# Optimization experiments

Hardware: AMD Instinct MI355X
Metric: run time of the kernel (lower is better)

## Reference

```python
import jax, jax.numpy as jnp
import numpy as np
from jax import lax

T, B, H, HID = 1024, 64, 512, 512
EPS = 1e-5


def _lstm_scan(xs, Wx, Wh, b):
    # xs: [T, B, H] time-major; returns hidden states [T, B, HID]
    bsz = xs.shape[1]
    c0 = jnp.zeros((bsz, Wh.shape[0]), xs.dtype)
    h0 = jnp.zeros_like(c0)

    def step(carry, x):
        c, h = carry
        z = x @ Wx + h @ Wh + b  # [B, 4*HID]
        i, f, g, o = jnp.split(z, 4, axis=-1)  # flax gate order i, f, g, o
        c = jax.nn.sigmoid(f) * c + jax.nn.sigmoid(i) * jnp.tanh(g)
        h = jax.nn.sigmoid(o) * jnp.tanh(c)
        return (c, h), h

    _, hs = lax.scan(step, (c0, h0), xs)
    return hs


def _flip_sequences(x_bth, lengths):
    # x_bth: [B, T, H]; keep padding at the end while reversing valid prefix.
    max_len = x_bth.shape[1]
    return jax.vmap(lambda x, l: jnp.flip(jnp.roll(x, max_len - l, axis=0), axis=0))(
        x_bth, lengths)


def setup_inputs() -> dict:
    key = jax.random.key(0)
    ks = jax.random.split(key, 12)
    inputs = jax.random.normal(ks[0], (T, B, H), jnp.float32)
    lengths = jax.random.randint(ks[1], (B,), T // 2, T + 1).astype(jnp.int32)
    t_idx = jnp.arange(T)[:, None]
    mask = (t_idx < lengths[None, :]).astype(jnp.float32).reshape(T * B, 1)
    # BatchNorm params
    scale = 1.0 + 0.1 * jax.random.normal(ks[2], (H,), jnp.float32)
    bias = 0.1 * jax.random.normal(ks[3], (H,), jnp.float32)
    sx = 1.0 / np.sqrt(H)
    sh = 1.0 / np.sqrt(HID)
    Wx_f = sx * jax.random.normal(ks[4], (H, 4 * HID), jnp.float32)
    Wh_f = sh * jax.random.normal(ks[5], (HID, 4 * HID), jnp.float32)
    b_f = jnp.zeros((4 * HID,), jnp.float32)
    Wx_b = sx * jax.random.normal(ks[6], (H, 4 * HID), jnp.float32)
    Wh_b = sh * jax.random.normal(ks[7], (HID, 4 * HID), jnp.float32)
    b_b = jnp.zeros((4 * HID,), jnp.float32)
    return {
        "inputs": inputs, "lengths": lengths, "mask": mask,
        "scale": scale, "bias": bias,
        "Wx_f": Wx_f, "Wh_f": Wh_f, "b_f": b_f,
        "Wx_b": Wx_b, "Wh_b": Wh_b, "b_b": b_b,
        "training": 1,
    }


def reference(inputs, lengths, mask, scale, bias,
              Wx_f, Wh_f, b_f, Wx_b, Wh_b, b_b, training):
    t, n, h = inputs.shape
    x = inputs.reshape(t * n, h)
    if training:
        # masked batch statistics (matches flax BatchNorm override)
        non_zeros = jnp.sum(mask, axis=0)  # [1]
        mean = jnp.sum(x, axis=0) / non_zeros  # [H]
        mean2 = jnp.sum(lax.square(x), axis=0) / non_zeros
        var = jnp.maximum(0.0, mean2 - lax.square(mean))
    else:
        mean = jnp.zeros((h,), jnp.float32)
        var = jnp.ones((h,), jnp.float32)
    y = (x - mean) * lax.rsqrt(var + EPS) * scale + bias
    y = (y * mask).reshape(t, n, h)  # [T, B, H]

    # forward direction
    fwd = _lstm_scan(y, Wx_f, Wh_f, b_f)  # [T, B, HID]
    # backward direction on length-aware flipped inputs
    rev_in = _flip_sequences(y.transpose(1, 0, 2), lengths).transpose(1, 0, 2)
    bwd = _lstm_scan(rev_in, Wx_b, Wh_b, b_b)
    bwd = _flip_sequences(bwd.transpose(1, 0, 2), lengths).transpose(1, 0, 2)
    return fwd + bwd  # [T, B, HID]
```

## Files before the change

### kernel.cpp

```cpp
#include <hip/hip_runtime.h>
#include <math.h>

#define T_DIM 1024
#define B_DIM 64
#define H_DIM 512
#define HID   512
#define EPS_F 1e-5f

#define WS_SUM    0
#define WS_SUMSQ  512
#define WS_A      1024
#define WS_C0     1536
#define WS_HBUF   4096
#define WS_CBUF   (4096 + 131072)
#define WS_XZ     (4096 + 131072 + 65536)
#define WS_END    (WS_XZ + 524288)

__device__ __forceinline__ float sigf(float v) {
    return 1.0f / (1.0f + __expf(-v));
}

__global__ void stats_kernel(const float* __restrict__ x, float* __restrict__ ws) {
    int col = blockIdx.x * 256 + threadIdx.x;
    int row0 = blockIdx.y * 512;
    float s = 0.f, s2 = 0.f;
    for (int r = 0; r < 512; ++r) {
        float v = x[(size_t)(row0 + r) * H_DIM + col];
        s += v;
        s2 += v * v;
    }
    atomicAdd(&ws[WS_SUM + col], s);
    atomicAdd(&ws[WS_SUMSQ + col], s2);
}

__global__ void finalize_kernel(const int* __restrict__ lengths,
                                const float* __restrict__ scale,
                                const float* __restrict__ bias,
                                const int* __restrict__ training,
                                float* __restrict__ ws) {
    __shared__ float cnt_sh;
    int tid = threadIdx.x;
    if (tid == 0) {
        int c = 0;
        for (int b = 0; b < B_DIM; ++b) c += lengths[b];
        cnt_sh = (float)c;
    }
    __syncthreads();
    float a, c0;
    if (*training) {
        float inv = 1.0f / cnt_sh;
        float mean = ws[WS_SUM + tid] * inv;
        float mean2 = ws[WS_SUMSQ + tid] * inv;
        float var = fmaxf(0.0f, mean2 - mean * mean);
        a = scale[tid] * rsqrtf(var + EPS_F);
        c0 = bias[tid] - mean * a;
    } else {
        a = scale[tid] * rsqrtf(1.0f + EPS_F);
        c0 = bias[tid];
    }
    ws[WS_A + tid] = a;
    ws[WS_C0 + tid] = c0;
}

__launch_bounds__(256)
__global__ void step_kernel(int t,
                            const float* __restrict__ x,
                            const int* __restrict__ lengths,
                            const float* __restrict__ mask,
                            const float* __restrict__ Wx_f, const float* __restrict__ Wh_f,
                            const float* __restrict__ b_f,
                            const float* __restrict__ Wx_b, const float* __restrict__ Wh_b,
                            const float* __restrict__ b_b,
                            float* __restrict__ ws, float* __restrict__ out) {
    __shared__ __align__(16) float As[64 * 68];
    __shared__ __align__(16) float Ws_[64 * 68];

    const int role = blockIdx.x >> 6;
    const int r6   = blockIdx.x & 63;
    const int dir  = r6 >> 5;
    const int jt   = r6 & 31;
    const int tid  = threadIdx.x;
    const int tidb = tid & 15;
    const int tidn = tid >> 4;
    const int b0   = tidb << 2;
    const int n0   = tidn << 2;

    const int target = t + 1;
    if (role == 0 && t < 0) return;
    if (role == 1 && target >= T_DIM) return;

    const int g   = tidn >> 2;
    const int jj0 = (tidn & 3) << 2;
    const int col_base = g * 512 + jt * 16 + jj0;

    const float* W  = (role == 1) ? (dir ? Wx_b : Wx_f) : (dir ? Wh_b : Wh_f);
    const float* bv = dir ? b_b : b_f;

    float acc[4][4];
    if (role == 0) {
        const int xzb = ((t & 1) * 2 + dir) * (B_DIM * 2048);
#pragma unroll
        for (int i = 0; i < 4; ++i) {
            float4 v = *reinterpret_cast<const float4*>(&ws[WS_XZ + xzb + (b0 + i) * 2048 + col_base]);
            acc[i][0] = v.x; acc[i][1] = v.y; acc[i][2] = v.z; acc[i][3] = v.w;
        }
    } else {
        float4 bvv = *reinterpret_cast<const float4*>(&bv[col_base]);
#pragma unroll
        for (int i = 0; i < 4; ++i) {
            acc[i][0] = bvv.x; acc[i][1] = bvv.y; acc[i][2] = bvv.z; acc[i][3] = bvv.w;
        }
    }

    const int hbase_in = ((t & 1) * 2 + dir) * (B_DIM * 512);

    for (int ck = 0; ck < 8; ++ck) {
        const int k0c = ck * 64;
#pragma unroll
        for (int i = 0; i < 4; ++i) {
            int f4  = tid + i * 256;
            int kk4 = f4 & 15;
            int b   = f4 >> 4;
            int k   = k0c + (kk4 << 2);
            float4 v;
            if (role == 0) {
                v = *reinterpret_cast<const float4*>(&ws[WS_HBUF + hbase_in + b * 512 + k]);
            } else {
                int trow;
                if (dir == 0) {
                    trow = target;
                } else {
                    trow = lengths[b] - 1 - target;
                    if (trow < 0) trow += T_DIM;
                }
                float4 xv = *reinterpret_cast<const float4*>(&x[((size_t)trow * B_DIM + b) * H_DIM + k]);
                float  m  = mask[(size_t)trow * B_DIM + b];
                float4 av = *reinterpret_cast<const float4*>(&ws[WS_A + k]);
                float4 cv = *reinterpret_cast<const float4*>(&ws[WS_C0 + k]);
                v.x = (xv.x * av.x + cv.x) * m;
                v.y = (xv.y * av.y + cv.y) * m;
                v.z = (xv.z * av.z + cv.z) * m;
                v.w = (xv.w * av.w + cv.w) * m;
            }
            int kr = kk4 << 2;
            As[(kr + 0) * 68 + b] = v.x;
            As[(kr + 1) * 68 + b] = v.y;
            As[(kr + 2) * 68 + b] = v.z;
            As[(kr + 3) * 68 + b] = v.w;
        }
#pragma unroll
        for (int i = 0; i < 4; ++i) {
            int f4  = tid + i * 256;
            int n4  = f4 & 15;
            int kk  = f4 >> 4;
            int nl  = n4 << 2;
            int gg  = nl >> 4;
            int jj  = nl & 15;
            int colw = gg * 512 + jt * 16 + jj;
            float4 wv = *reinterpret_cast<const float4*>(&W[(size_t)(k0c + kk) * 2048 + colw]);
            *reinterpret_cast<float4*>(&Ws_[kk * 68 + nl]) = wv;
        }
        __syncthreads();
#pragma unroll 4
        for (int kk = 0; kk < 64; ++kk) {
            const float4 a4 = *reinterpret_cast<const float4*>(&As[kk * 68 + b0]);
            const float4 w4 = *reinterpret_cast<const float4*>(&Ws_[kk * 68 + n0]);
            acc[0][0] += a4.x * w4.x; acc[0][1] += a4.x * w4.y; acc[0][2] += a4.x * w4.z; acc[0][3] += a4.x * w4.w;
            acc[1][0] += a4.y * w4.x; acc[1][1] += a4.y * w4.y; acc[1][2] += a4.y * w4.z; acc[1][3] += a4.y * w4.w;
            acc[2][0] += a4.z * w4.x; acc[2][1] += a4.z * w4.y; acc[2][2] += a4.z * w4.z; acc[2][3] += a4.z * w4.w;
            acc[3][0] += a4.w * w4.x; acc[3][1] += a4.w * w4.y; acc[3][2] += a4.w * w4.z; acc[3][3] += a4.w * w4.w;
        }
        __syncthreads();
    }

    if (role == 1) {
        const int xzb = ((target & 1) * 2 + dir) * (B_DIM * 2048);
#pragma unroll
        for (int i = 0; i < 4; ++i) {
            float4 v = make_float4(acc[i][0], acc[i][1], acc[i][2], acc[i][3]);
            *reinterpret_cast<float4*>(&ws[WS_XZ + xzb + (b0 + i) * 2048 + col_base]) = v;
        }
        return;
    }

    float* zs = As;
#pragma unroll
    for (int i = 0; i < 4; ++i) {
        float4 v = make_float4(acc[i][0], acc[i][1], acc[i][2], acc[i][3]);
        *reinterpret_cast<float4*>(&zs[(b0 + i) * 68 + n0]) = v;
    }
    __syncthreads();

    const int b   = tid >> 2;
    const int jjg = (tid & 3) << 2;
    const int hc  = jt * 16 + jjg;

    float4 zi = *reinterpret_cast<const float4*>(&zs[b * 68 +  0 + jjg]);
    float4 zf = *reinterpret_cast<const float4*>(&zs[b * 68 + 16 + jjg]);
    float4 zg = *reinterpret_cast<const float4*>(&zs[b * 68 + 32 + jjg]);
    float4 zo = *reinterpret_cast<const float4*>(&zs[b * 68 + 48 + jjg]);

    float* cptr = &ws[WS_CBUF + (dir * B_DIM + b) * 512 + hc];
    float4 c4 = *reinterpret_cast<const float4*>(cptr);

    float cn[4], hv[4];
    {
        float c = sigf(zf.x) * c4.x + sigf(zi.x) * tanhf(zg.x);
        cn[0] = c; hv[0] = sigf(zo.x) * tanhf(c);
    }
    {
        float c = sigf(zf.y) * c4.y + sigf(zi.y) * tanhf(zg.y);
        cn[1] = c; hv[1] = sigf(zo.y) * tanhf(c);
    }
    {
        float c = sigf(zf.z) * c4.z + sigf(zi.z) * tanhf(zg.z);
        cn[2] = c; hv[2] = sigf(zo.z) * tanhf(c);
    }
    {
        float c = sigf(zf.w) * c4.w + sigf(zi.w) * tanhf(zg.w);
        cn[3] = c; hv[3] = sigf(zo.w) * tanhf(c);
    }

    *reinterpret_cast<float4*>(cptr) = make_float4(cn[0], cn[1], cn[2], cn[3]);

    const int hbase_out = (((t + 1) & 1) * 2 + dir) * (B_DIM * 512);
    *reinterpret_cast<float4*>(&ws[WS_HBUF + hbase_out + b * 512 + hc]) =
        make_float4(hv[0], hv[1], hv[2], hv[3]);

    int orow;
    if (dir == 0) {
        orow = t;
    } else {
        orow = lengths[b] - 1 - t;
        if (orow < 0) orow += T_DIM;
    }
    float* op = &out[((size_t)orow * B_DIM + b) * HID + hc];
    atomicAdd(&op[0], hv[0]);
    atomicAdd(&op[1], hv[1]);
    atomicAdd(&op[2], hv[2]);
    atomicAdd(&op[3], hv[3]);
}

extern "C" void kernel_launch(void* const* d_in, const int* in_sizes, int n_in,
                              void* d_out, int out_size, void* d_ws, size_t ws_size,
                              hipStream_t stream) {
    const float* x        = (const float*)d_in[0];
    const int*   lengths  = (const int*)d_in[1];
    const float* mask     = (const float*)d_in[2];
    const float* scale    = (const float*)d_in[3];
    const float* bias     = (const float*)d_in[4];
    const float* Wx_f     = (const float*)d_in[5];
    const float* Wh_f     = (const float*)d_in[6];
    const float* b_f      = (const float*)d_in[7];
    const float* Wx_b     = (const float*)d_in[8];
    const float* Wh_b     = (const float*)d_in[9];
    const float* b_b      = (const float*)d_in[10];
    const int*   training = (const int*)d_in[11];
    float* ws  = (float*)d_ws;
    float* out = (float*)d_out;

    hipMemsetAsync(ws, 0, (size_t)WS_END * sizeof(float), stream);
    hipMemsetAsync(out, 0, (size_t)out_size * sizeof(float), stream);

    stats_kernel<<<dim3(2, 128), 256, 0, stream>>>(x, ws);
    finalize_kernel<<<1, 512, 0, stream>>>(lengths, scale, bias, training, ws);

    for (int t = -1; t < T_DIM; ++t) {
        step_kernel<<<128, 256, 0, stream>>>(t, x, lengths, mask,
                                             Wx_f, Wh_f, b_f, Wx_b, Wh_b, b_b,
                                             ws, out);
    }
}
```

Baseline: 40.19 ms.

## Restructure LSTM step kernel with async LDS staging and batch-major layout

Rewrites the per-timestep kernel so each of 256 blocks owns 8 hidden columns across all four gates and all 64 batch rows. Each lane handles one batch row, the activation/input tile is double-buffered into LDS via global_load_lds, and weights are read directly from global memory rather than staged. The BatchNorm shift term is folded algebraically into a precomputed Wx·c0 vector, and h, c and xz are stored in transposed layouts for coalesced access. The out memset size changes from elements to bytes, which looks like a bug that leaves most of the output uncleared before the atomic adds.

```diff
diff --git a/kernel.cpp b/kernel.cpp
--- a/kernel.cpp
+++ b/kernel.cpp
@@ -11,14 +11,22 @@
 #define WS_SUMSQ  512
 #define WS_A      1024
 #define WS_C0     1536
-#define WS_HBUF   4096
-#define WS_CBUF   (4096 + 131072)
-#define WS_XZ     (4096 + 131072 + 65536)
+#define WS_CVEC   2048
+#define WS_CST    (2048 + 4096)
+#define WS_H      (WS_CST + 65536)
+#define WS_XZ     (WS_H + 131072)
 #define WS_END    (WS_XZ + 524288)
+
+#define H_PAR     65536
+#define XZ_PAR    262144
 
 __device__ __forceinline__ float sigf(float v) {
     return 1.0f / (1.0f + __expf(-v));
 }
+
+#define ASYNC_CP16(gp, lp) \
+    __builtin_amdgcn_global_load_lds((__attribute__((address_space(1))) void*)(gp), \
+                                     (__attribute__((address_space(3))) void*)(lp), 16, 0, 0)
 
 __global__ void stats_kernel(const float* __restrict__ x, float* __restrict__ ws) {
     int col = blockIdx.x * 256 + threadIdx.x;
@@ -62,183 +70,171 @@
     ws[WS_C0 + tid] = c0;
 }
 
+__global__ void cvec_kernel(const float* __restrict__ Wx_f, const float* __restrict__ Wx_b,
+                            float* __restrict__ ws) {
+    const int n = blockIdx.x * 256 + threadIdx.x;
+    const float* c0 = ws + WS_C0;
+    float s0 = 0.f, s1 = 0.f;
+    for (int k = 0; k < 512; ++k) {
+        const float c = c0[k];
+        s0 += c * Wx_f[(size_t)k * 2048 + n];
+        s1 += c * Wx_b[(size_t)k * 2048 + n];
+    }
+    ws[WS_CVEC + n] = s0;
+    ws[WS_CVEC + 2048 + n] = s1;
+}
+
 __launch_bounds__(256)
 __global__ void step_kernel(int t,
                             const float* __restrict__ x,
                             const int* __restrict__ lengths,
                             const float* __restrict__ mask,
-                            const float* __restrict__ Wx_f, const float* __restrict__ Wh_f,
-                            const float* __restrict__ b_f,
-                            const float* __restrict__ Wx_b, const float* __restrict__ Wh_b,
-                            const float* __restrict__ b_b,
-                            float* __restrict__ ws, float* __restrict__ out) {
-    __shared__ __align__(16) float As[64 * 68];
-    __shared__ __align__(16) float Ws_[64 * 68];
-
-    const int role = blockIdx.x >> 6;
-    const int r6   = blockIdx.x & 63;
-    const int dir  = r6 >> 5;
-    const int jt   = r6 & 31;
+                            const float* __restrict__ Wh_f, const float* __restrict__ Wh_b,
+                            const float* __restrict__ Wx_f, const float* __restrict__ Wx_b,
+                            const float* __restrict__ b_f,  const float* __restrict__ b_b,
+                            const float* __restrict__ abn,
+                            const float* __restrict__ cvec,
+                            const float* __restrict__ h_r,
+                            float*       __restrict__ h_w,
+                            const float* __restrict__ xz_r,
+                            float*       __restrict__ xz_w,
+                            float*       __restrict__ cst,
+                            float*       __restrict__ out) {
     const int tid  = threadIdx.x;
-    const int tidb = tid & 15;
-    const int tidn = tid >> 4;
-    const int b0   = tidb << 2;
-    const int n0   = tidn << 2;
-
+    const int lane = tid & 63;
+    const int wid  = __builtin_amdgcn_readfirstlane(tid >> 6);
+    const int role = blockIdx.x >> 7;
+    const int bid7 = blockIdx.x & 127;
+    const int dir  = bid7 >> 6;
+    const int blk  = bid7 & 63;
+    const int hcbase = blk << 3;
     const int target = t + 1;
+
     if (role == 0 && t < 0) return;
     if (role == 1 && target >= T_DIM) return;
 
-    const int g   = tidn >> 2;
-    const int jj0 = (tidn & 3) << 2;
-    const int col_base = g * 512 + jt * 16 + jj0;
-
-    const float* W  = (role == 1) ? (dir ? Wx_b : Wx_f) : (dir ? Wh_b : Wh_f);
-    const float* bv = dir ? b_b : b_f;
-
-    float acc[4][4];
+    __shared__ __align__(16) float buf[2][8192];
+    __shared__ __align__(16) float zs[2048];
+
+    const int nbase = (wid << 9) + hcbase;
+
+    float acc[8];
+#pragma unroll
+    for (int j = 0; j < 8; ++j) acc[j] = 0.f;
+
     if (role == 0) {
-        const int xzb = ((t & 1) * 2 + dir) * (B_DIM * 2048);
-#pragma unroll
-        for (int i = 0; i < 4; ++i) {
-            float4 v = *reinterpret_cast<const float4*>(&ws[WS_XZ + xzb + (b0 + i) * 2048 + col_base]);
-            acc[i][0] = v.x; acc[i][1] = v.y; acc[i][2] = v.z; acc[i][3] = v.w;
+        const float* W = dir ? Wh_b : Wh_f;
+        const float* hsrc = h_r + dir * 32768;
+#pragma unroll
+        for (int ii = 0; ii < 8; ++ii) {
+            int i = (wid << 3) + ii;
+            ASYNC_CP16(hsrc + i * 256 + lane * 4, &buf[0][i * 256]);
+        }
+        __syncthreads();
+        for (int c = 0; c < 4; ++c) {
+            if (c < 3) {
+                const float* src = hsrc + (c + 1) * 8192;
+                float* db = &buf[(c + 1) & 1][0];
+#pragma unroll
+                for (int ii = 0; ii < 8; ++ii) {
+                    int i = (wid << 3) + ii;
+                    ASYNC_CP16(src + i * 256 + lane * 4, db + i * 256);
+                }
+            }
+            const float* bcur = &buf[c & 1][0];
+            const int kg0 = c << 7;
+#pragma unroll 4
+            for (int q = 0; q < 32; ++q) {
+                float4 a4 = *reinterpret_cast<const float4*>(&bcur[(q << 8) + (lane << 2)]);
+                const float* wr = W + (size_t)(kg0 + (q << 2)) * 2048 + nbase;
+#pragma unroll
+                for (int j = 0; j < 8; ++j) acc[j] = fmaf(a4.x, wr[j], acc[j]);
+#pragma unroll
+                for (int j = 0; j < 8; ++j) acc[j] = fmaf(a4.y, wr[2048 + j], acc[j]);
+#pragma unroll
+                for (int j = 0; j < 8; ++j) acc[j] = fmaf(a4.z, wr[4096 + j], acc[j]);
+#pragma unroll
+                for (int j = 0; j < 8; ++j) acc[j] = fmaf(a4.w, wr[6144 + j], acc[j]);
+            }
+            if (c < 3) __syncthreads();
+        }
+#pragma unroll
+        for (int j = 0; j < 8; ++j)
+            zs[((wid << 3) + j) * 64 + lane] = acc[j];
+        __syncthreads();
+
+        const int b  = tid & 63;
+        const int jj = tid >> 6;
+#pragma unroll
+        for (int u = 0; u < 2; ++u) {
+            const int jx = (jj << 1) + u;
+            const int hc = hcbase + jx;
+            const float zi = zs[(jx << 6) + b]        + xz_r[((dir << 11) + hc) * 64 + b];
+            const float zf = zs[((8 + jx) << 6) + b]  + xz_r[((dir << 11) + 512 + hc) * 64 + b];
+            const float zg = zs[((16 + jx) << 6) + b] + xz_r[((dir << 11) + 1024 + hc) * 64 + b];
+            const float zo = zs[((24 + jx) << 6) + b] + xz_r[((dir << 11) + 1536 + hc) * 64 + b];
+            float* cp = &cst[((dir << 9) + hc) * 64 + b];
+            const float cold = *cp;
+            const float cn = sigf(zf) * cold + sigf(zi) * tanhf(zg);
+            *cp = cn;
+            const float hv = sigf(zo) * tanhf(cn);
+            h_w[dir * 32768 + (((hc >> 2) << 6) + b) * 4 + (hc & 3)] = hv;
+            int orow;
+            if (dir == 0) orow = t;
+            else { orow = lengths[b] - 1 - t; if (orow < 0) orow += T_DIM; }
+            atomicAdd(&out[((size_t)orow * B_DIM + b) * HID + hc], hv);
         }
     } else {
-        float4 bvv = *reinterpret_cast<const float4*>(&bv[col_base]);
-#pragma unroll
-        for (int i = 0; i < 4; ++i) {
-            acc[i][0] = bvv.x; acc[i][1] = bvv.y; acc[i][2] = bvv.z; acc[i][3] = bvv.w;
-        }
-    }
-
-    const int hbase_in = ((t & 1) * 2 + dir) * (B_DIM * 512);
-
-    for (int ck = 0; ck < 8; ++ck) {
-        const int k0c = ck * 64;
-#pragma unroll
-        for (int i = 0; i < 4; ++i) {
-            int f4  = tid + i * 256;
-            int kk4 = f4 & 15;
-            int b   = f4 >> 4;
-            int k   = k0c + (kk4 << 2);
-            float4 v;
-            if (role == 0) {
-                v = *reinterpret_cast<const float4*>(&ws[WS_HBUF + hbase_in + b * 512 + k]);
-            } else {
-                int trow;
-                if (dir == 0) {
-                    trow = target;
-                } else {
-                    trow = lengths[b] - 1 - target;
-                    if (trow < 0) trow += T_DIM;
+        const float* W = dir ? Wx_b : Wx_f;
+        int trow;
+        if (dir == 0) trow = target;
+        else { trow = lengths[lane] - 1 - target; if (trow < 0) trow += T_DIM; }
+        const float* xsrc = x + ((size_t)trow * B_DIM + lane) * H_DIM;
+#pragma unroll
+        for (int ii = 0; ii < 8; ++ii) {
+            int i = (wid << 3) + ii;
+            ASYNC_CP16(xsrc + i * 4, &buf[0][i * 256]);
+        }
+        __syncthreads();
+        for (int c = 0; c < 4; ++c) {
+            if (c < 3) {
+                const float* src = xsrc + (c + 1) * 128;
+                float* db = &buf[(c + 1) & 1][0];
+#pragma unroll
+                for (int ii = 0; ii < 8; ++ii) {
+                    int i = (wid << 3) + ii;
+                    ASYNC_CP16(src + i * 4, db + i * 256);
                 }
-                float4 xv = *reinterpret_cast<const float4*>(&x[((size_t)trow * B_DIM + b) * H_DIM + k]);
-                float  m  = mask[(size_t)trow * B_DIM + b];
-                float4 av = *reinterpret_cast<const float4*>(&ws[WS_A + k]);
-                float4 cv = *reinterpret_cast<const float4*>(&ws[WS_C0 + k]);
-                v.x = (xv.x * av.x + cv.x) * m;
-                v.y = (xv.y * av.y + cv.y) * m;
-                v.z = (xv.z * av.z + cv.z) * m;
-                v.w = (xv.w * av.w + cv.w) * m;
-            }
-            int kr = kk4 << 2;
-            As[(kr + 0) * 68 + b] = v.x;
-            As[(kr + 1) * 68 + b] = v.y;
-            As[(kr + 2) * 68 + b] = v.z;
-            As[(kr + 3) * 68 + b] = v.w;
-        }
-#pragma unroll
-        for (int i = 0; i < 4; ++i) {
-            int f4  = tid + i * 256;
-            int n4  = f4 & 15;
-            int kk  = f4 >> 4;
-            int nl  = n4 << 2;
-            int gg  = nl >> 4;
-            int jj  = nl & 15;
-            int colw = gg * 512 + jt * 16 + jj;
-            float4 wv = *reinterpret_cast<const float4*>(&W[(size_t)(k0c + kk) * 2048 + colw]);
-            *reinterpret_cast<float4*>(&Ws_[kk * 68 + nl]) = wv;
-        }
-        __syncthreads();
+            }
+            const float* bcur = &buf[c & 1][0];
+            const int kg0 = c << 7;
 #pragma unroll 4
-        for (int kk = 0; kk < 64; ++kk) {
-            const float4 a4 = *reinterpret_cast<const float4*>(&As[kk * 68 + b0]);
-            const float4 w4 = *reinterpret_cast<const float4*>(&Ws_[kk * 68 + n0]);
-            acc[0][0] += a4.x * w4.x; acc[0][1] += a4.x * w4.y; acc[0][2] += a4.x * w4.z; acc[0][3] += a4.x * w4.w;
-            acc[1][0] += a4.y * w4.x; acc[1][1] += a4.y * w4.y; acc[1][2] += a4.y * w4.z; acc[1][3] += a4.y * w4.w;
-            acc[2][0] += a4.z * w4.x; acc[2][1] += a4.z * w4.y; acc[2][2] += a4.z * w4.z; acc[2][3] += a4.z * w4.w;
-            acc[3][0] += a4.w * w4.x; acc[3][1] += a4.w * w4.y; acc[3][2] += a4.w * w4.z; acc[3][3] += a4.w * w4.w;
-        }
-        __syncthreads();
-    }
-
-    if (role == 1) {
-        const int xzb = ((target & 1) * 2 + dir) * (B_DIM * 2048);
-#pragma unroll
-        for (int i = 0; i < 4; ++i) {
-            float4 v = make_float4(acc[i][0], acc[i][1], acc[i][2], acc[i][3]);
-            *reinterpret_cast<float4*>(&ws[WS_XZ + xzb + (b0 + i) * 2048 + col_base]) = v;
-        }
-        return;
-    }
-
-    float* zs = As;
-#pragma unroll
-    for (int i = 0; i < 4; ++i) {
-        float4 v = make_float4(acc[i][0], acc[i][1], acc[i][2], acc[i][3]);
-        *reinterpret_cast<float4*>(&zs[(b0 + i) * 68 + n0]) = v;
-    }
-    __syncthreads();
-
-    const int b   = tid >> 2;
-    const int jjg = (tid & 3) << 2;
-    const int hc  = jt * 16 + jjg;
-
-    float4 zi = *reinterpret_cast<const float4*>(&zs[b * 68 +  0 + jjg]);
-    float4 zf = *reinterpret_cast<const float4*>(&zs[b * 68 + 16 + jjg]);
-    float4 zg = *reinterpret_cast<const float4*>(&zs[b * 68 + 32 + jjg]);
-    float4 zo = *reinterpret_cast<const float4*>(&zs[b * 68 + 48 + jjg]);
-
-    float* cptr = &ws[WS_CBUF + (dir * B_DIM + b) * 512 + hc];
-    float4 c4 = *reinterpret_cast<const float4*>(cptr);
-
-    float cn[4], hv[4];
-    {
-        float c = sigf(zf.x) * c4.x + sigf(zi.x) * tanhf(zg.x);
-        cn[0] = c; hv[0] = sigf(zo.x) * tanhf(c);
-    }
-    {
-        float c = sigf(zf.y) * c4.y + sigf(zi.y) * tanhf(zg.y);
-        cn[1] = c; hv[1] = sigf(zo.y) * tanhf(c);
-    }
-    {
-        float c = sigf(zf.z) * c4.z + sigf(zi.z) * tanhf(zg.z);
-        cn[2] = c; hv[2] = sigf(zo.z) * tanhf(c);
-    }
-    {
-        float c = sigf(zf.w) * c4.w + sigf(zi.w) * tanhf(zg.w);
-        cn[3] = c; hv[3] = sigf(zo.w) * tanhf(c);
-    }
-
-    *reinterpret_cast<float4*>(cptr) = make_float4(cn[0], cn[1], cn[2], cn[3]);
-
-    const int hbase_out = (((t + 1) & 1) * 2 + dir) * (B_DIM * 512);
-    *reinterpret_cast<float4*>(&ws[WS_HBUF + hbase_out + b * 512 + hc]) =
-        make_float4(hv[0], hv[1], hv[2], hv[3]);
-
-    int orow;
-    if (dir == 0) {
-        orow = t;
-    } else {
-        orow = lengths[b] - 1 - t;
-        if (orow < 0) orow += T_DIM;
-    }
-    float* op = &out[((size_t)orow * B_DIM + b) * HID + hc];
-    atomicAdd(&op[0], hv[0]);
-    atomicAdd(&op[1], hv[1]);
-    atomicAdd(&op[2], hv[2]);
-    atomicAdd(&op[3], hv[3]);
+            for (int q = 0; q < 32; ++q) {
+                float4 a4 = *reinterpret_cast<const float4*>(&bcur[(q << 8) + (lane << 2)]);
+                const int kg = kg0 + (q << 2);
+                const float4 av = *reinterpret_cast<const float4*>(&abn[kg]);
+                a4.x *= av.x; a4.y *= av.y; a4.z *= av.z; a4.w *= av.w;
+                const float* wr = W + (size_t)kg * 2048 + nbase;
+#pragma unroll
+                for (int j = 0; j < 8; ++j) acc[j] = fmaf(a4.x, wr[j], acc[j]);
+#pragma unroll
+                for (int j = 0; j < 8; ++j) acc[j] = fmaf(a4.y, wr[2048 + j], acc[j]);
+#pragma unroll
+                for (int j = 0; j < 8; ++j) acc[j] = fmaf(a4.z, wr[4096 + j], acc[j]);
+#pragma unroll
+                for (int j = 0; j < 8; ++j) acc[j] = fmaf(a4.w, wr[6144 + j], acc[j]);
+            }
+            if (c < 3) __syncthreads();
+        }
+        const float m = mask[(size_t)trow * B_DIM + lane];
+        const float* bv = dir ? b_b : b_f;
+#pragma unroll
+        for (int j = 0; j < 8; ++j) {
+            const int n = nbase + j;
+            const float v = m * (acc[j] + cvec[(dir << 11) + n]) + bv[n];
+            xz_w[((dir << 11) + n) * 64 + lane] = v;
+        }
+    }
 }
 
 extern "C" void kernel_launch(void* const* d_in, const int* in_sizes, int n_in,
@@ -260,14 +256,20 @@
     float* out = (float*)d_out;
 
     hipMemsetAsync(ws, 0, (size_t)WS_END * sizeof(float), stream);
-    hipMemsetAsync(out, 0, (size_t)out_size * sizeof(float), stream);
+    hipMemsetAsync(out, 0, (size_t)out_size, stream);
 
     stats_kernel<<<dim3(2, 128), 256, 0, stream>>>(x, ws);
     finalize_kernel<<<1, 512, 0, stream>>>(lengths, scale, bias, training, ws);
+    cvec_kernel<<<8, 256, 0, stream>>>(Wx_f, Wx_b, ws);
 
     for (int t = -1; t < T_DIM; ++t) {
-        step_kernel<<<128, 256, 0, stream>>>(t, x, lengths, mask,
-                                             Wx_f, Wh_f, b_f, Wx_b, Wh_b, b_b,
-                                             ws, out);
-    }
-}
+        const int pr = t & 1;
+        const int pw = (t + 1) & 1;
+        step_kernel<<<256, 256, 0, stream>>>(t, x, lengths, mask,
+            Wh_f, Wh_b, Wx_f, Wx_b, b_f, b_b,
+            ws + WS_A, ws + WS_CVEC,
+            ws + WS_H + pr * H_PAR,   ws + WS_H + pw * H_PAR,
+            ws + WS_XZ + pr * XZ_PAR, ws + WS_XZ + pw * XZ_PAR,
+            ws + WS_CST, out);
+    }
+}
```

After: 47.15 ms. 1.17x slower.
